# Performance work log

Measured on AMD Instinct MI355X. Metric: run time of the kernel, lower is better.

Reference implementation:

```python
import jax, jax.numpy as jnp
import numpy as np
from jax import lax

DIM = 384
HEADS = 8
HEAD_DIM = DIM // HEADS
EPS = 1e-06


def setup_inputs() -> dict:
    key = jax.random.key(0)
    ks = jax.random.split(key, 16)
    B, N, C = 8, 4096, DIM
    s = 0.02
    inp = {
        "x": jax.random.normal(ks[0], (B, N, C), jnp.float32),
        "wq": jax.random.normal(ks[1], (C, C), jnp.float32) * s,
        "bq": jnp.zeros((C,), jnp.float32),
        "wk": jax.random.normal(ks[2], (C, C), jnp.float32) * s,
        "bk": jnp.zeros((C,), jnp.float32),
        "wv": jax.random.normal(ks[3], (C, C), jnp.float32) * s,
        "bv": jnp.zeros((C,), jnp.float32),
        "wg": jax.random.normal(ks[4], (C, C), jnp.float32) * s,
        "bg": jnp.zeros((C,), jnp.float32),
        "wo": jax.random.normal(ks[5], (C, C), jnp.float32) * s,
        "bo": jnp.zeros((C,), jnp.float32),
        "temperature": jnp.ones((HEADS, 1, 1), jnp.float32),
        "dw_w": jax.random.normal(ks[6], (C, 1, 3, 3), jnp.float32) * s,  # depthwise 3x3
        "dw_b": jnp.zeros((C,), jnp.float32),
        "pw_w": jax.random.normal(ks[7], (C, C), jnp.float32) * s,        # pointwise 1x1
        "pw_b": jnp.zeros((C,), jnp.float32),
    }
    return inp


def _phi(x):
    # exp(x - max) over last dim, numerically stable
    return jnp.exp(x - jnp.max(x, axis=-1, keepdims=True))


def _token_mixer(x, dw_w, dw_b, pw_w, pw_b):
    B, N, C = x.shape
    H = W = int(np.sqrt(N))
    feat = x.transpose(0, 2, 1).reshape(B, C, H, W)
    feat = lax.conv_general_dilated(
        feat, dw_w, window_strides=(1, 1), padding=((1, 1), (1, 1)),
        feature_group_count=C, dimension_numbers=("NCHW", "OIHW", "NCHW"))
    feat = feat + dw_b[None, :, None, None]
    feat = jnp.einsum("bchw,oc->bohw", feat, pw_w) + pw_b[None, :, None, None]
    return feat.reshape(B, C, N).transpose(0, 2, 1)


def reference(x, wq, bq, wk, bk, wv, bv, wg, bg, wo, bo, temperature,
              dw_w, dw_b, pw_w, pw_b):
    B, N, C = x.shape
    residual = x
    x = x + _token_mixer(x, dw_w, dw_b, pw_w, pw_b)

    def heads(y):  # [B,N,C] -> [B,H,N,d]
        return y.reshape(B, N, HEADS, HEAD_DIM).transpose(0, 2, 1, 3)

    q = heads(jnp.einsum("bnc,oc->bno", x, wq) + bq)
    k = heads(jnp.einsum("bnc,oc->bno", x, wk) + bk)
    v = heads(jnp.einsum("bnc,oc->bno", x, wv) + bv)
    g = heads(jnp.einsum("bnc,oc->bno", x, wg) + bg)

    q = _phi(q * temperature[None])       # temperature: [H,1,1] broadcasts over [B,H,N,d]
    k = _phi(k)
    v = v * jax.nn.sigmoid(g)

    kv = jnp.einsum("bhnd,bhne->bhde", k, v)     # [B,H,d,d]
    k_sum = jnp.sum(k, axis=2)                   # [B,H,d]
    num = jnp.einsum("bhnd,bhde->bhne", q, kv)   # [B,H,N,d]
    den = jnp.einsum("bhnd,bhd->bhn", q, k_sum)[..., None] + EPS
    out = num / den

    out = out.transpose(0, 2, 1, 3).reshape(B, N, C)
    out = jnp.einsum("bnc,oc->bno", out, wo) + bo
    return out + 0.0 * residual
```

## Files before the change

### kernel.cpp

```cpp
#include <hip/hip_runtime.h>
#include <math.h>

#define EPSF 1e-6f

typedef __attribute__((ext_vector_type(8))) short bf16x8;
typedef __attribute__((ext_vector_type(4))) float f32x4;
typedef unsigned short u16;
typedef unsigned int u32;

#define MFMA16(a,b,c) __builtin_amdgcn_mfma_f32_16x16x32_bf16((a),(b),(c),0,0,0)

__device__ __forceinline__ u16 f2bf(float f){
  u32 x = __builtin_bit_cast(u32, f);
  u32 r = (x + 0x7fffu + ((x >> 16) & 1u)) >> 16;
  return (u16)r;
}
__device__ __forceinline__ void gll16(const void* g, void* l){
  __builtin_amdgcn_global_load_lds(
      (const __attribute__((address_space(1))) u32*)g,
      (__attribute__((address_space(3))) u32*)l, 16, 0, 0);
}

__global__ __launch_bounds__(256) void k0_prep(
    const float* __restrict__ wq, const float* __restrict__ bq,
    const float* __restrict__ wk, const float* __restrict__ bk,
    const float* __restrict__ wv, const float* __restrict__ bv,
    const float* __restrict__ wg, const float* __restrict__ bg,
    const float* __restrict__ pw_w, const float* __restrict__ wo,
    u16* __restrict__ wpack, u16* __restrict__ pwb, u16* __restrict__ wob,
    float* __restrict__ bpack)
{
  int idx = blockIdx.x*256 + threadIdx.x;
  const int NW = 1536*384;
  if (idx < NW) {
    int r = idx / 384, c = idx - r*384;
    int h = r / 192, s = (r % 192)/48, d = r % 48;
    const float* w = (s==0)?wq:(s==1)?wk:(s==2)?wv:wg;
    wpack[idx] = f2bf(w[(h*48+d)*384 + c]);
    if (c==0){
      const float* b = (s==0)?bq:(s==1)?bk:(s==2)?bv:bg;
      bpack[r] = b[h*48+d];
    }
  } else if (idx < NW + 147456) {
    pwb[idx - NW] = f2bf(pw_w[idx - NW]);
  } else if (idx < NW + 2*147456) {
    wob[idx - NW - 147456] = f2bf(wo[idx - NW - 147456]);
  }
}

__global__ __launch_bounds__(256) void k1_dw(
    const float* __restrict__ x, const float* __restrict__ dw_w,
    const float* __restrict__ dw_b, u16* __restrict__ t)
{
  int idx = blockIdx.x*256 + threadIdx.x;
  int c4 = idx % 96; int rest = idx / 96;
  int jg = rest & 15; rest >>= 4;
  int i = rest & 63; int b = rest >> 6;
  int c0 = c4*4, j0 = jg*4;
  float wf[36];
  {
    const float4* wp = (const float4*)(dw_w + c0*9);
    #pragma unroll
    for (int k=0;k<9;k++){
      float4 v = wp[k];
      wf[4*k] = v.x; wf[4*k+1] = v.y; wf[4*k+2] = v.z; wf[4*k+3] = v.w;
    }
  }
  float4 bias = *(const float4*)(dw_b + c0);
  float acc[4][4];
  #pragma unroll
  for (int tk=0;tk<4;tk++){
    acc[tk][0]=bias.x; acc[tk][1]=bias.y; acc[tk][2]=bias.z; acc[tk][3]=bias.w;
  }
  const float* xb = x + ((size_t)b<<12)*384;
  #pragma unroll
  for (int di=-1; di<=1; ++di){
    int ii = i+di; if ((unsigned)ii >= 64u) continue;
    #pragma unroll
    for (int dj=-1; dj<=4; ++dj){
      int jj = j0+dj; if ((unsigned)jj >= 64u) continue;
      float4 xv = *(const float4*)(xb + (size_t)((ii<<6)+jj)*384 + c0);
      #pragma unroll
      for (int tk=0;tk<4;tk++){
        const int dd = dj - tk;
        if (dd < -1 || dd > 1) continue;
        const int tap = (di+1)*3 + (dd+1);
        acc[tk][0] = fmaf(xv.x, wf[0*9+tap], acc[tk][0]);
        acc[tk][1] = fmaf(xv.y, wf[1*9+tap], acc[tk][1]);
        acc[tk][2] = fmaf(xv.z, wf[2*9+tap], acc[tk][2]);
        acc[tk][3] = fmaf(xv.w, wf[3*9+tap], acc[tk][3]);
      }
    }
  }
  int mbase = (b<<12) + (i<<6) + j0;
  #pragma unroll
  for (int tk=0;tk<4;tk++){
    ushort4 o; o.x=f2bf(acc[tk][0]); o.y=f2bf(acc[tk][1]);
    o.z=f2bf(acc[tk][2]); o.w=f2bf(acc[tk][3]);
    *(ushort4*)(t + (size_t)(mbase+tk)*384 + c0) = o;
  }
}

__global__ __launch_bounds__(256) void k2_gemm_pw(
    const u16* __restrict__ t, const u16* __restrict__ pwb,
    const float* __restrict__ x, const float* __restrict__ pw_b,
    u16* __restrict__ xm)
{
  __shared__ __align__(16) u16 smem[32768];
  const int m0 = blockIdx.x * 128;
  const int n0 = blockIdx.y * 128;
  const int tid = threadIdx.x, w = tid>>6, l = tid&63;
  const int lc = l & 15, hi = l >> 4;
  const int osw = ((l&7) ^ (l>>3))*16;
  const f32x4 zf = {0.f,0.f,0.f,0.f};
  f32x4 acc[4][4];
  #pragma unroll
  for (int i=0;i<4;i++)
    #pragma unroll
    for (int j=0;j<4;j++) acc[i][j] = zf;

  const int srow = (w*4)*8 + (l>>3);

  #define K2_STAGE(T, BUF) do {                                            \
    const int k0_ = (T)*64;                                                \
    char* Ab_ = (char*)(smem + (BUF)*8192);                                \
    char* Bb_ = (char*)(smem + 16384 + (BUF)*8192);                        \
    _Pragma("unroll")                                                      \
    for (int i=0;i<4;i++){                                                 \
      gll16((const char*)t   + ((size_t)(m0+srow+i*8)*384 + k0_)*2 + osw,  \
            Ab_ + (w*4+i)*1024);                                           \
      gll16((const char*)pwb + ((size_t)(n0+srow+i*8)*384 + k0_)*2 + osw,  \
            Bb_ + (w*4+i)*1024);                                           \
    }                                                                      \
  } while(0)

  K2_STAGE(0, 0);
  __syncthreads();
  int cur = 0;
  for (int t_=0; t_<6; ++t_){
    if (t_ < 5) K2_STAGE(t_+1, cur^1);
    const u16* As = smem + cur*8192;
    const u16* Bs = smem + 16384 + cur*8192;
    const int wr = (w>>1)*64, wc = (w&1)*64;
    #pragma unroll
    for (int kk=0; kk<64; kk+=32){
      const int sc = (((kk>>3)+hi) ^ (lc&7))*8;
      bf16x8 a[4], bb[4];
      #pragma unroll
      for (int i=0;i<4;i++) a[i]  = *(const bf16x8*)&As[(wr + i*16 + lc)*64 + sc];
      #pragma unroll
      for (int j=0;j<4;j++) bb[j] = *(const bf16x8*)&Bs[(wc + j*16 + lc)*64 + sc];
      #pragma unroll
      for (int i=0;i<4;i++)
        #pragma unroll
        for (int j=0;j<4;j++)
          acc[i][j] = MFMA16(a[i], bb[j], acc[i][j]);
    }
    __syncthreads();
    cur ^= 1;
  }
  #undef K2_STAGE
  const int wr=(w>>1)*64, wc=(w&1)*64;
  #pragma unroll
  for (int j=0;j<4;j++){
    int n = n0 + wc + j*16 + lc;
    float bias = pw_b[n];
    #pragma unroll
    for (int i=0;i<4;i++)
      #pragma unroll
      for (int r=0;r<4;r++){
        int m = m0 + wr + i*16 + hi*4 + r;
        float v = acc[i][j][r] + x[(size_t)m*384 + n] + bias;
        xm[(size_t)m*384 + n] = f2bf(v);
      }
  }
}

__global__ __launch_bounds__(256) void k3_gemm_qkvg(
    const u16* __restrict__ xm, const u16* __restrict__ wpack,
    const float* __restrict__ bpack, const float* __restrict__ temperature,
    u16* __restrict__ qh, float* __restrict__ pkv, float* __restrict__ pks)
{
  __shared__ __align__(16) u16 smem[40960];
  const int m0 = blockIdx.x * 128;
  const int h  = blockIdx.y;
  const int tid = threadIdx.x, w = tid>>6, l = tid&63;
  const int lc = l & 15, hi = l >> 4;
  const int osw = ((l&7) ^ (l>>3))*16;
  const f32x4 zf = {0.f,0.f,0.f,0.f};
  f32x4 acc[2][12];
  #pragma unroll
  for (int i=0;i<2;i++)
    #pragma unroll
    for (int j=0;j<12;j++) acc[i][j] = zf;

  const int arow = (w*4)*8 + (l>>3);
  const int brow = (w*6)*8 + (l>>3);

  #define K3_STAGE(T, BUF) do {                                                \
    const int k0_ = (T)*64;                                                    \
    char* Ab_ = (char*)(smem + (BUF)*8192);                                    \
    char* Bb_ = (char*)(smem + 16384 + (BUF)*12288);                           \
    _Pragma("unroll")                                                          \
    for (int i=0;i<4;i++)                                                      \
      gll16((const char*)xm + ((size_t)(m0+arow+i*8)*384 + k0_)*2 + osw,       \
            Ab_ + (w*4+i)*1024);                                               \
    _Pragma("unroll")                                                          \
    for (int i=0;i<6;i++)                                                      \
      gll16((const char*)wpack + ((size_t)(h*192+brow+i*8)*384 + k0_)*2 + osw, \
            Bb_ + (w*6+i)*1024);                                               \
  } while(0)

  K3_STAGE(0, 0);
  __syncthreads();
  int cur = 0;
  const int rbase = w*32;
  for (int t=0; t<6; ++t){
    if (t < 5) K3_STAGE(t+1, cur^1);
    const u16* Ab = smem + cur*8192;
    const u16* Bb = smem + 16384 + cur*12288;
    #pragma unroll
    for (int kk=0; kk<64; kk+=32){
      const int sc = (((kk>>3)+hi) ^ (lc&7))*8;
      bf16x8 a0 = *(const bf16x8*)&Ab[(rbase +      lc)*64 + sc];
      bf16x8 a1 = *(const bf16x8*)&Ab[(rbase + 16 + lc)*64 + sc];
      #pragma unroll
      for (int j=0;j<12;j++){
        bf16x8 bb = *(const bf16x8*)&Bb[(j*16 + lc)*64 + sc];
        acc[0][j] = MFMA16(a0, bb, acc[0][j]);
        acc[1][j] = MFMA16(a1, bb, acc[1][j]);
      }
    }
    __syncthreads();
    cur ^= 1;
  }
  #undef K3_STAGE

  const float tq = temperature[h];
  const int b = m0 >> 12;
  const int mtile = (m0 >> 7) & 31;
  const size_t bh = (size_t)b*8 + h;
  const int bb0 = h*192;
  float biasq[3], biask[3], biasv[3], biasg[3];
  #pragma unroll
  for (int j=0;j<3;j++){
    biasq[j] = bpack[bb0       + j*16 + lc];
    biask[j] = bpack[bb0 + 48  + j*16 + lc];
    biasv[j] = bpack[bb0 + 96  + j*16 + lc];
    biasg[j] = bpack[bb0 + 144 + j*16 + lc];
  }
  u16* kT = smem;
  u16* vT = smem + 6528;
  float ksp[3] = {0.f, 0.f, 0.f};

  #pragma unroll
  for (int i=0;i<2;i++){
    ushort4 kst[3], vst[3];
    #pragma unroll
    for (int r=0;r<4;r++){
      int m = m0 + w*32 + i*16 + hi*4 + r;
      int n = m & 4095;
      size_t rowq = (bh*4096 + n)*48;
      float q0=(acc[i][0][r]+biasq[0])*tq;
      float q1=(acc[i][1][r]+biasq[1])*tq;
      float q2=(acc[i][2][r]+biasq[2])*tq;
      qh[rowq +      lc] = f2bf(__expf(q0));
      qh[rowq + 16 + lc] = f2bf(__expf(q1));
      qh[rowq + 32 + lc] = f2bf(__expf(q2));
      float s0=acc[i][3][r]+biask[0];
      float s1=acc[i][4][r]+biask[1];
      float s2=acc[i][5][r]+biask[2];
      float mk = fmaxf(s0,fmaxf(s1,s2));
      mk = fmaxf(mk, __shfl_xor(mk,1,64));
      mk = fmaxf(mk, __shfl_xor(mk,2,64));
      mk = fmaxf(mk, __shfl_xor(mk,4,64));
      mk = fmaxf(mk, __shfl_xor(mk,8,64));
      float k0e = __expf(s0-mk), k1e = __expf(s1-mk), k2e = __expf(s2-mk);
      ksp[0] += k0e; ksp[1] += k1e; ksp[2] += k2e;
      u16 kq0=f2bf(k0e), kq1=f2bf(k1e), kq2=f2bf(k2e);
      u16 vq[3];
      #pragma unroll
      for (int j=0;j<3;j++){
        float vv = acc[i][6+j][r] + biasv[j];
        float gg = acc[i][9+j][r] + biasg[j];
        float sg = __builtin_amdgcn_rcpf(1.f + __expf(-gg));
        vq[j] = f2bf(vv*sg);
      }
      if (r==0){ kst[0].x=kq0; kst[1].x=kq1; kst[2].x=kq2; vst[0].x=vq[0]; vst[1].x=vq[1]; vst[2].x=vq[2]; }
      if (r==1){ kst[0].y=kq0; kst[1].y=kq1; kst[2].y=kq2; vst[0].y=vq[0]; vst[1].y=vq[1]; vst[2].y=vq[2]; }
      if (r==2){ kst[0].z=kq0; kst[1].z=kq1; kst[2].z=kq2; vst[0].z=vq[0]; vst[1].z=vq[1]; vst[2].z=vq[2]; }
      if (r==3){ kst[0].w=kq0; kst[1].w=kq1; kst[2].w=kq2; vst[0].w=vq[0]; vst[1].w=vq[1]; vst[2].w=vq[2]; }
    }
    int mb = w*32 + i*16 + hi*4;
    #pragma unroll
    for (int j=0;j<3;j++){
      *(ushort4*)&kT[(j*16+lc)*136 + mb] = kst[j];
      *(ushort4*)&vT[(j*16+lc)*136 + mb] = vst[j];
    }
  }
  __syncthreads();

  bf16x8 af[3], bfv[3];
  #pragma unroll
  for (int da=0;da<3;da++) af[da]  = *(const bf16x8*)&kT[(da*16+lc)*136 + w*32 + hi*8];
  #pragma unroll
  for (int eb=0;eb<3;eb++) bfv[eb] = *(const bf16x8*)&vT[(eb*16+lc)*136 + w*32 + hi*8];
  f32x4 a2[3][3];
  #pragma unroll
  for (int da=0;da<3;da++)
    #pragma unroll
    for (int eb=0;eb<3;eb++)
      a2[da][eb] = MFMA16(af[da], bfv[eb], zf);
  __syncthreads();
  float* pb = (float*)smem + w*2304;
  #pragma unroll
  for (int da=0;da<3;da++)
    #pragma unroll
    for (int eb=0;eb<3;eb++)
      #pragma unroll
      for (int rr=0;rr<4;rr++)
        pb[(da*16 + hi*4 + rr)*48 + eb*16 + lc] = a2[da][eb][rr];
  __syncthreads();
  {
    float* p0 = (float*)smem;
    float* dst = pkv + ((size_t)bh*32 + mtile)*2304;
    for (int u=tid; u<2304; u+=256)
      dst[u] = p0[u] + p0[2304+u] + p0[4608+u] + p0[6912+u];
  }
  #pragma unroll
  for (int j=0;j<3;j++){
    ksp[j] += __shfl_xor(ksp[j],16,64);
    ksp[j] += __shfl_xor(ksp[j],32,64);
  }
  __syncthreads();
  {
    float* kr = (float*)smem;
    if (hi==0){ kr[w*48+lc]=ksp[0]; kr[w*48+16+lc]=ksp[1]; kr[w*48+32+lc]=ksp[2]; }
    __syncthreads();
    if (tid < 48){
      float* ds = pks + ((size_t)bh*32 + mtile)*48;
      ds[tid] = kr[tid] + kr[48+tid] + kr[96+tid] + kr[144+tid];
    }
  }
}

__global__ __launch_bounds__(256) void k5_red(
    const float* __restrict__ pkv, const float* __restrict__ pks,
    u16* __restrict__ kvp)
{
  __shared__ float sm[2304];
  __shared__ float ks[48];
  int bh = blockIdx.x, tid = threadIdx.x;
  const float* base = pkv + (size_t)bh*32*2304;
  for (int u=tid; u<2304; u+=256){
    float v = 0.f;
    #pragma unroll
    for (int m=0;m<32;m++) v += base[(size_t)m*2304 + u];
    sm[u] = v;
  }
  if (tid < 48){
    const float* bk = pks + (size_t)bh*32*48 + tid;
    float v = 0.f;
    #pragma unroll
    for (int m=0;m<32;m++) v += bk[m*48];
    ks[tid] = v;
  }
  __syncthreads();
  for (int u=tid; u<4096; u+=256){
    int e = u >> 6, d = u & 63;
    float v = 0.f;
    if (e < 48 && d < 48)       v = sm[d*48 + e];
    else if (e == 48 && d < 48) v = ks[d];
    kvp[((size_t)bh*64 + e)*64 + d] = f2bf(v);
  }
}

__global__ __launch_bounds__(256) void k6_num(
    const u16* __restrict__ qh, const u16* __restrict__ kvp, u16* __restrict__ ah)
{
  __shared__ __align__(16) u16 As[256*64];
  __shared__ __align__(16) u16 Bs[64*64];
  const int bh = blockIdx.x >> 4, nc = blockIdx.x & 15;
  const int tid = threadIdx.x, w = tid>>6, l = tid&63;
  const int lc = l & 15, hi = l >> 4;
  const f32x4 zf = {0.f,0.f,0.f,0.f};
  const uint4 z4 = {0,0,0,0};
  const u16* gq = qh + ((size_t)bh*4096 + nc*256)*48;
  #pragma unroll
  for (int it=0; it<8; ++it){
    int s = it*256 + tid;
    int row = s>>3, c = s&7, g = c ^ (row&7);
    ((uint4*)As)[s] = (g < 6) ? *(const uint4*)(gq + (size_t)row*48 + g*8) : z4;
  }
  const u16* gk = kvp + (size_t)bh*4096;
  #pragma unroll
  for (int it=0; it<2; ++it){
    int s = it*256 + tid;
    int row = s>>3, c = s&7, g = c ^ (row&7);
    ((uint4*)Bs)[s] = *(const uint4*)(gk + (size_t)row*64 + g*8);
  }
  __syncthreads();
  f32x4 acc[4][4];
  #pragma unroll
  for (int i=0;i<4;i++)
    #pragma unroll
    for (int j=0;j<4;j++) acc[i][j] = zf;
  const int rbase = w*64;
  #pragma unroll
  for (int kk=0; kk<64; kk+=32){
    const int sc = (((kk>>3)+hi) ^ (lc&7))*8;
    bf16x8 a[4], bb[4];
    #pragma unroll
    for (int i=0;i<4;i++) a[i]  = *(const bf16x8*)&As[(rbase + i*16 + lc)*64 + sc];
    #pragma unroll
    for (int j=0;j<4;j++) bb[j] = *(const bf16x8*)&Bs[(j*16 + lc)*64 + sc];
    #pragma unroll
    for (int i=0;i<4;i++)
      #pragma unroll
      for (int j=0;j<4;j++)
        acc[i][j] = MFMA16(a[i], bb[j], acc[i][j]);
  }
  const int b = bh >> 3, h = bh & 7;
  #pragma unroll
  for (int i=0;i<4;i++){
    #pragma unroll
    for (int r=0;r<4;r++){
      float den = __shfl(acc[i][3][r], l & 48, 64) + EPSF;
      float rd = __builtin_amdgcn_rcpf(den);
      int n = nc*256 + rbase + i*16 + hi*4 + r;
      size_t ob = ((size_t)b*4096 + n)*384 + h*48;
      ah[ob +      lc] = f2bf(acc[i][0][r]*rd);
      ah[ob + 16 + lc] = f2bf(acc[i][1][r]*rd);
      ah[ob + 32 + lc] = f2bf(acc[i][2][r]*rd);
    }
  }
}

__global__ __launch_bounds__(256) void k7_gemm_out(
    const u16* __restrict__ ah, const u16* __restrict__ wob,
    const float* __restrict__ bo, float* __restrict__ out)
{
  __shared__ __align__(16) u16 smem[32768];
  const int m0 = blockIdx.x * 128;
  const int n0 = blockIdx.y * 128;
  const int tid = threadIdx.x, w = tid>>6, l = tid&63;
  const int lc = l & 15, hi = l >> 4;
  const int osw = ((l&7) ^ (l>>3))*16;
  const f32x4 zf = {0.f,0.f,0.f,0.f};
  f32x4 acc[4][4];
  #pragma unroll
  for (int i=0;i<4;i++)
    #pragma unroll
    for (int j=0;j<4;j++) acc[i][j] = zf;

  const int srow = (w*4)*8 + (l>>3);

  #define K7_STAGE(T, BUF) do {                                            \
    const int k0_ = (T)*64;                                                \
    char* Ab_ = (char*)(smem + (BUF)*8192);                                \
    char* Bb_ = (char*)(smem + 16384 + (BUF)*8192);                        \
    _Pragma("unroll")                                                      \
    for (int i=0;i<4;i++){                                                 \
      gll16((const char*)ah  + ((size_t)(m0+srow+i*8)*384 + k0_)*2 + osw,  \
            Ab_ + (w*4+i)*1024);                                           \
      gll16((const char*)wob + ((size_t)(n0+srow+i*8)*384 + k0_)*2 + osw,  \
            Bb_ + (w*4+i)*1024);                                           \
    }                                                                      \
  } while(0)

  K7_STAGE(0, 0);
  __syncthreads();
  int cur = 0;
  for (int t_=0; t_<6; ++t_){
    if (t_ < 5) K7_STAGE(t_+1, cur^1);
    const u16* As = smem + cur*8192;
    const u16* Bs = smem + 16384 + cur*8192;
    const int wr = (w>>1)*64, wc = (w&1)*64;
    #pragma unroll
    for (int kk=0; kk<64; kk+=32){
      const int sc = (((kk>>3)+hi) ^ (lc&7))*8;
      bf16x8 a[4], bb[4];
      #pragma unroll
      for (int i=0;i<4;i++) a[i]  = *(const bf16x8*)&As[(wr + i*16 + lc)*64 + sc];
      #pragma unroll
      for (int j=0;j<4;j++) bb[j] = *(const bf16x8*)&Bs[(wc + j*16 + lc)*64 + sc];
      #pragma unroll
      for (int i=0;i<4;i++)
        #pragma unroll
        for (int j=0;j<4;j++)
          acc[i][j] = MFMA16(a[i], bb[j], acc[i][j]);
    }
    __syncthreads();
    cur ^= 1;
  }
  #undef K7_STAGE
  const int wr=(w>>1)*64, wc=(w&1)*64;
  #pragma unroll
  for (int j=0;j<4;j++){
    int n = n0 + wc + j*16 + lc;
    float bias = bo[n];
    #pragma unroll
    for (int i=0;i<4;i++)
      #pragma unroll
      for (int r=0;r<4;r++){
        int m = m0 + wr + i*16 + hi*4 + r;
        out[(size_t)m*384 + n] = acc[i][j][r] + bias;
      }
  }
}

extern "C" void kernel_launch(void* const* d_in, const int* in_sizes, int n_in,
                              void* d_out, int out_size, void* d_ws, size_t ws_size,
                              hipStream_t stream)
{
  const float* x    = (const float*)d_in[0];
  const float* wq   = (const float*)d_in[1];
  const float* bq   = (const float*)d_in[2];
  const float* wk   = (const float*)d_in[3];
  const float* bk   = (const float*)d_in[4];
  const float* wv   = (const float*)d_in[5];
  const float* bv   = (const float*)d_in[6];
  const float* wg   = (const float*)d_in[7];
  const float* bg   = (const float*)d_in[8];
  const float* wo   = (const float*)d_in[9];
  const float* bo   = (const float*)d_in[10];
  const float* temp = (const float*)d_in[11];
  const float* dw_w = (const float*)d_in[12];
  const float* dw_b = (const float*)d_in[13];
  const float* pw_w = (const float*)d_in[14];
  const float* pw_b = (const float*)d_in[15];
  float* out = (float*)d_out;
  char* ws = (char*)d_ws;

  u16*   t       = (u16*)(ws + 0);
  float* pkv     = (float*)(ws + 0);
  float* pks     = (float*)(ws + 18874368);
  u16*   ah      = (u16*)(ws + 0);
  u16*   xm      = (u16*)(ws + 25165824);
  u16*   qh      = (u16*)(ws + 50331648);
  u16*   wpack   = (u16*)(ws + 83886080);
  u16*   pwb     = (u16*)(ws + 85065728);
  u16*   wob     = (u16*)(ws + 85360640);
  float* bpack   = (float*)(ws + 85655552);
  u16*   kvp     = (u16*)(ws + 85661696);

  k0_prep<<<3456, 256, 0, stream>>>(wq,bq,wk,bk,wv,bv,wg,bg,pw_w,wo,
                                    wpack,pwb,wob,bpack);
  k1_dw<<<3072, 256, 0, stream>>>(x, dw_w, dw_b, t);
  k2_gemm_pw<<<dim3(256,3), 256, 0, stream>>>(t, pwb, x, pw_b, xm);
  k3_gemm_qkvg<<<dim3(256,8), 256, 0, stream>>>(xm, wpack, bpack, temp, qh, pkv, pks);
  k5_red<<<64, 256, 0, stream>>>(pkv, pks, kvp);
  k6_num<<<1024, 256, 0, stream>>>(qh, kvp, ah);
  k7_gemm_out<<<dim3(256,3), 256, 0, stream>>>(ah, wob, bo, out);
}
```

Measured before the change: 174.6 us.

## Fuse per-head numerator/normalization into output projection GEMM via LDS

Merges the per-head q·kv numerator kernel with the output projection GEMM. Each 128x128 output tile loops over the 8 heads, computing the normalized attention output for its 128 rows into shared memory and immediately multiplying it by the matching 48-column slice of wo. This removes the bf16 round trip of the attention output through global memory and one kernel launch. In exchange, each head's numerator is recomputed once for each of the three column tiles, the K dimension is padded from 48 to 64 per head, and the async double-buffered pipeline is replaced by synchronous loads with three barriers per head.

Result: slower. 195.9 us (+12.1%).

```diff
diff --git a/kernel.cpp b/kernel.cpp
--- a/kernel.cpp
+++ b/kernel.cpp
@@ -375,125 +375,114 @@
   }
 }
 
-__global__ __launch_bounds__(256) void k6_num(
-    const u16* __restrict__ qh, const u16* __restrict__ kvp, u16* __restrict__ ah)
-{
-  __shared__ __align__(16) u16 As[256*64];
-  __shared__ __align__(16) u16 Bs[64*64];
-  const int bh = blockIdx.x >> 4, nc = blockIdx.x & 15;
+__global__ __launch_bounds__(256) void k67_fused(
+    const u16* __restrict__ qh, const u16* __restrict__ kvp,
+    const u16* __restrict__ wob, const float* __restrict__ bo,
+    float* __restrict__ out)
+{
+  __shared__ __align__(16) u16 q_lds[128*64];
+  __shared__ __align__(16) u16 kv_lds[64*64];
+  __shared__ __align__(16) u16 ah_lds[128*64];
+  __shared__ __align__(16) u16 wo_lds[128*64];
+  const int m0 = blockIdx.x * 128;
+  const int n0 = blockIdx.y * 128;
   const int tid = threadIdx.x, w = tid>>6, l = tid&63;
   const int lc = l & 15, hi = l >> 4;
   const f32x4 zf = {0.f,0.f,0.f,0.f};
   const uint4 z4 = {0,0,0,0};
-  const u16* gq = qh + ((size_t)bh*4096 + nc*256)*48;
-  #pragma unroll
-  for (int it=0; it<8; ++it){
-    int s = it*256 + tid;
-    int row = s>>3, c = s&7, g = c ^ (row&7);
-    ((uint4*)As)[s] = (g < 6) ? *(const uint4*)(gq + (size_t)row*48 + g*8) : z4;
-  }
-  const u16* gk = kvp + (size_t)bh*4096;
-  #pragma unroll
-  for (int it=0; it<2; ++it){
-    int s = it*256 + tid;
-    int row = s>>3, c = s&7, g = c ^ (row&7);
-    ((uint4*)Bs)[s] = *(const uint4*)(gk + (size_t)row*64 + g*8);
-  }
-  __syncthreads();
-  f32x4 acc[4][4];
+  const int b = m0 >> 12;
+  const int nbase = m0 & 4095;
+
+  #pragma unroll
+  for (int it=0; it<4; ++it) ((uint4*)ah_lds)[it*256 + tid] = z4;
+
+  f32x4 acc_o[4][4];
   #pragma unroll
   for (int i=0;i<4;i++)
     #pragma unroll
-    for (int j=0;j<4;j++) acc[i][j] = zf;
-  const int rbase = w*64;
-  #pragma unroll
-  for (int kk=0; kk<64; kk+=32){
-    const int sc = (((kk>>3)+hi) ^ (lc&7))*8;
-    bf16x8 a[4], bb[4];
-    #pragma unroll
-    for (int i=0;i<4;i++) a[i]  = *(const bf16x8*)&As[(rbase + i*16 + lc)*64 + sc];
-    #pragma unroll
-    for (int j=0;j<4;j++) bb[j] = *(const bf16x8*)&Bs[(j*16 + lc)*64 + sc];
-    #pragma unroll
-    for (int i=0;i<4;i++)
-      #pragma unroll
-      for (int j=0;j<4;j++)
-        acc[i][j] = MFMA16(a[i], bb[j], acc[i][j]);
-  }
-  const int b = bh >> 3, h = bh & 7;
-  #pragma unroll
-  for (int i=0;i<4;i++){
-    #pragma unroll
-    for (int r=0;r<4;r++){
-      float den = __shfl(acc[i][3][r], l & 48, 64) + EPSF;
-      float rd = __builtin_amdgcn_rcpf(den);
-      int n = nc*256 + rbase + i*16 + hi*4 + r;
-      size_t ob = ((size_t)b*4096 + n)*384 + h*48;
-      ah[ob +      lc] = f2bf(acc[i][0][r]*rd);
-      ah[ob + 16 + lc] = f2bf(acc[i][1][r]*rd);
-      ah[ob + 32 + lc] = f2bf(acc[i][2][r]*rd);
-    }
-  }
-}
-
-__global__ __launch_bounds__(256) void k7_gemm_out(
-    const u16* __restrict__ ah, const u16* __restrict__ wob,
-    const float* __restrict__ bo, float* __restrict__ out)
-{
-  __shared__ __align__(16) u16 smem[32768];
-  const int m0 = blockIdx.x * 128;
-  const int n0 = blockIdx.y * 128;
-  const int tid = threadIdx.x, w = tid>>6, l = tid&63;
-  const int lc = l & 15, hi = l >> 4;
-  const int osw = ((l&7) ^ (l>>3))*16;
-  const f32x4 zf = {0.f,0.f,0.f,0.f};
-  f32x4 acc[4][4];
-  #pragma unroll
-  for (int i=0;i<4;i++)
-    #pragma unroll
-    for (int j=0;j<4;j++) acc[i][j] = zf;
-
-  const int srow = (w*4)*8 + (l>>3);
-
-  #define K7_STAGE(T, BUF) do {                                            \
-    const int k0_ = (T)*64;                                                \
-    char* Ab_ = (char*)(smem + (BUF)*8192);                                \
-    char* Bb_ = (char*)(smem + 16384 + (BUF)*8192);                        \
-    _Pragma("unroll")                                                      \
-    for (int i=0;i<4;i++){                                                 \
-      gll16((const char*)ah  + ((size_t)(m0+srow+i*8)*384 + k0_)*2 + osw,  \
-            Ab_ + (w*4+i)*1024);                                           \
-      gll16((const char*)wob + ((size_t)(n0+srow+i*8)*384 + k0_)*2 + osw,  \
-            Bb_ + (w*4+i)*1024);                                           \
-    }                                                                      \
-  } while(0)
-
-  K7_STAGE(0, 0);
-  __syncthreads();
-  int cur = 0;
-  for (int t_=0; t_<6; ++t_){
-    if (t_ < 5) K7_STAGE(t_+1, cur^1);
-    const u16* As = smem + cur*8192;
-    const u16* Bs = smem + 16384 + cur*8192;
+    for (int j=0;j<4;j++) acc_o[i][j] = zf;
+
+  for (int h = 0; h < 8; ++h){
+    const size_t bh = (size_t)b*8 + h;
+    {
+      const u16* gq = qh + (bh*4096 + (size_t)nbase)*48;
+      #pragma unroll
+      for (int it=0; it<4; ++it){
+        int s = it*256 + tid;
+        int row = s>>3, c = s&7, g = c ^ (row&7);
+        ((uint4*)q_lds)[s] = (g < 6) ? *(const uint4*)(gq + (size_t)row*48 + g*8) : z4;
+      }
+      const u16* gk = kvp + bh*4096;
+      #pragma unroll
+      for (int it=0; it<2; ++it){
+        int s = it*256 + tid;
+        int row = s>>3, c = s&7, g = c ^ (row&7);
+        ((uint4*)kv_lds)[s] = *(const uint4*)(gk + (size_t)row*64 + g*8);
+      }
+      const u16* gw = wob + (size_t)n0*384 + h*48;
+      #pragma unroll
+      for (int it=0; it<4; ++it){
+        int s = it*256 + tid;
+        int row = s>>3, c = s&7, g = c ^ (row&7);
+        ((uint4*)wo_lds)[s] = (g < 6) ? *(const uint4*)(gw + (size_t)row*384 + g*8) : z4;
+      }
+    }
+    __syncthreads();
+
+    f32x4 aq[2][4];
+    #pragma unroll
+    for (int i=0;i<2;i++)
+      #pragma unroll
+      for (int j=0;j<4;j++) aq[i][j] = zf;
+    #pragma unroll
+    for (int kk=0; kk<64; kk+=32){
+      const int sc = (((kk>>3)+hi) ^ (lc&7))*8;
+      bf16x8 a0 = *(const bf16x8*)&q_lds[(w*32 +      lc)*64 + sc];
+      bf16x8 a1 = *(const bf16x8*)&q_lds[(w*32 + 16 + lc)*64 + sc];
+      bf16x8 bb[4];
+      #pragma unroll
+      for (int j=0;j<4;j++) bb[j] = *(const bf16x8*)&kv_lds[(j*16 + lc)*64 + sc];
+      #pragma unroll
+      for (int j=0;j<4;j++){
+        aq[0][j] = MFMA16(a0, bb[j], aq[0][j]);
+        aq[1][j] = MFMA16(a1, bb[j], aq[1][j]);
+      }
+    }
+    #pragma unroll
+    for (int i=0;i<2;i++){
+      #pragma unroll
+      for (int r=0;r<4;r++){
+        float den = __shfl(aq[i][3][r], l & 48, 64) + EPSF;
+        float rd = __builtin_amdgcn_rcpf(den);
+        int tr = w*32 + i*16 + hi*4 + r;
+        #pragma unroll
+        for (int j=0;j<3;j++){
+          int e = j*16 + lc;
+          int cslot = ((e>>3) ^ (tr&7))*8 + (e&7);
+          ah_lds[tr*64 + cslot] = f2bf(aq[i][j][r]*rd);
+        }
+      }
+    }
+    __syncthreads();
+
     const int wr = (w>>1)*64, wc = (w&1)*64;
     #pragma unroll
     for (int kk=0; kk<64; kk+=32){
       const int sc = (((kk>>3)+hi) ^ (lc&7))*8;
       bf16x8 a[4], bb[4];
       #pragma unroll
-      for (int i=0;i<4;i++) a[i]  = *(const bf16x8*)&As[(wr + i*16 + lc)*64 + sc];
-      #pragma unroll
-      for (int j=0;j<4;j++) bb[j] = *(const bf16x8*)&Bs[(wc + j*16 + lc)*64 + sc];
+      for (int i=0;i<4;i++) a[i]  = *(const bf16x8*)&ah_lds[(wr + i*16 + lc)*64 + sc];
+      #pragma unroll
+      for (int j=0;j<4;j++) bb[j] = *(const bf16x8*)&wo_lds[(wc + j*16 + lc)*64 + sc];
       #pragma unroll
       for (int i=0;i<4;i++)
         #pragma unroll
         for (int j=0;j<4;j++)
-          acc[i][j] = MFMA16(a[i], bb[j], acc[i][j]);
+          acc_o[i][j] = MFMA16(a[i], bb[j], acc_o[i][j]);
     }
     __syncthreads();
-    cur ^= 1;
-  }
-  #undef K7_STAGE
+  }
+
   const int wr=(w>>1)*64, wc=(w&1)*64;
   #pragma unroll
   for (int j=0;j<4;j++){
@@ -504,7 +493,7 @@
       #pragma unroll
       for (int r=0;r<4;r++){
         int m = m0 + wr + i*16 + hi*4 + r;
-        out[(size_t)m*384 + n] = acc[i][j][r] + bias;
+        out[(size_t)m*384 + n] = acc_o[i][j][r] + bias;
       }
   }
 }
@@ -535,7 +524,6 @@
   u16*   t       = (u16*)(ws + 0);
   float* pkv     = (float*)(ws + 0);
   float* pks     = (float*)(ws + 18874368);
-  u16*   ah      = (u16*)(ws + 0);
   u16*   xm      = (u16*)(ws + 25165824);
   u16*   qh      = (u16*)(ws + 50331648);
   u16*   wpack   = (u16*)(ws + 83886080);
@@ -550,6 +538,5 @@
   k2_gemm_pw<<<dim3(256,3), 256, 0, stream>>>(t, pwb, x, pw_b, xm);
   k3_gemm_qkvg<<<dim3(256,8), 256, 0, stream>>>(xm, wpack, bpack, temp, qh, pkv, pks);
   k5_red<<<64, 256, 0, stream>>>(pkv, pks, kvp);
-  k6_num<<<1024, 256, 0, stream>>>(qh, kvp, ah);
-  k7_gemm_out<<<dim3(256,3), 256, 0, stream>>>(ah, wob, bo, out);
-}
+  k67_fused<<<dim3(256,3), 256, 0, stream>>>(qh, kvp, wob, bo, out);
+}
```
